# Performance work log

Measured on AMD Instinct MI355X. Metric: run time of the kernel, lower is better.

The kernel has to match this reference:

```python
import jax, jax.numpy as jnp
import numpy as np

B, H, W = 32, 128, 128
NA = 9            # number of anchors
STRIDE = 16.0
CLS_THRESH = 0.95
MAX_IOU = 0.1
NUM_PROP = 10
NEG = -1e9        # sentinel for suppressed / below-threshold scores


def setup_inputs() -> dict:
    key = jax.random.key(0)
    inputs = jax.random.normal(key, (B, H, W, NA * 4 + NA + 1), dtype=jnp.float32)
    anchors = jnp.array([[0.5, 32.0], [1.0, 32.0], [2.0, 32.0],
                         [0.5, 64.0], [1.0, 64.0], [2.0, 64.0],
                         [0.5, 128.0], [1.0, 128.0], [2.0, 128.0]], dtype=jnp.float32)
    return {"inputs": inputs, "anchors": anchors}


def _decode(inputs, anchors):
    b, h, w, c = inputs.shape
    cls = inputs[..., -1]
    # zero out 1-pixel border (the tf.pad'ed cancel matrix)
    border = jnp.zeros((h, w), inputs.dtype).at[1:-1, 1:-1].set(1.0)
    cls = cls * border
    a_reg = inputs[..., -10:-1]           # [B,H,W,9]
    bbox_reg = inputs[..., :-10]          # [B,H,W,36]
    a_idx = jnp.argmax(a_reg, axis=-1)    # [B,H,W] best anchor per position
    # gather the 4 deltas of the chosen anchor: channels a_idx*4 .. a_idx*4+3
    gidx = a_idx[..., None] * 4 + jnp.arange(4)
    deltas = jnp.take_along_axis(bbox_reg, gidx, axis=-1)          # [B,H,W,4]
    anc = anchors[a_idx].astype(jnp.float32)                       # [B,H,W,2]
    # anchor box: center x from column, center y from row, height=anc[:,1], width=anc[:,1]/anc[:,0]
    ax = (jnp.arange(w, dtype=jnp.float32)[None, :] + 0.5) * STRIDE  # [1,W]
    ay = (jnp.arange(h, dtype=jnp.float32)[:, None] + 0.5) * STRIDE  # [H,1]
    a0 = jnp.broadcast_to(ax, (h, w))[None]                          # [1,H,W]
    a1 = jnp.broadcast_to(ay, (h, w))[None]
    a2 = anc[..., 1]
    a3 = anc[..., 1] / anc[..., 0]
    b0 = deltas[..., 0] * a2 + a0
    b1 = deltas[..., 1] * a3 + a1
    b2 = jnp.exp(deltas[..., 2]) * a2
    b3 = jnp.exp(deltas[..., 3]) * a3
    bboxes = jnp.stack([b0, b1, b2, b3], axis=-1)                    # [B,H,W,4]
    coords = jnp.stack([b1 - b3 / 2, b0 - b2 / 2,
                        b1 + b3 / 2, b0 + b2 / 2], axis=-1)          # [y1,x1,y2,x2]
    scores = jnp.where(cls > CLS_THRESH, cls, NEG)                   # mask below-threshold
    n = h * w
    return (bboxes.reshape(b, n, 4), coords.reshape(b, n, 4), scores.reshape(b, n))


def _nms_one(boxes, coords, scores):
    # greedy NMS, equivalent to tf.image.non_max_suppression over the valid candidates
    n = scores.shape[0]
    area = jnp.maximum(coords[:, 2] - coords[:, 0], 0.0) * jnp.maximum(coords[:, 3] - coords[:, 1], 0.0)
    idx_range = jnp.arange(n)

    def body(i, state):
        sc, out = state
        j = jnp.argmax(sc)
        ok = sc[j] > NEG / 2
        sel = coords[j]
        iy1 = jnp.maximum(coords[:, 0], sel[0])
        ix1 = jnp.maximum(coords[:, 1], sel[1])
        iy2 = jnp.minimum(coords[:, 2], sel[2])
        ix2 = jnp.minimum(coords[:, 3], sel[3])
        inter = jnp.maximum(iy2 - iy1, 0.0) * jnp.maximum(ix2 - ix1, 0.0)
        area_s = jnp.maximum(sel[2] - sel[0], 0.0) * jnp.maximum(sel[3] - sel[1], 0.0)
        iou = inter / (area + area_s - inter + 1e-10)
        suppress = (iou > MAX_IOU) | (idx_range == j)
        sc = jnp.where(ok & suppress, NEG, sc)
        out = out.at[i].set(jnp.where(ok, boxes[j], jnp.zeros(4, boxes.dtype)))
        return sc, out

    out0 = jnp.zeros((NUM_PROP, 4), boxes.dtype)
    _, out = jax.lax.fori_loop(0, NUM_PROP, body, (scores, out0))
    return out


def _forward(inputs, anchors):
    bboxes, coords, scores = _decode(inputs, anchors)
    return jax.vmap(_nms_one)(bboxes, coords, scores)   # [B, NUM_PROP, 4]


def reference(inputs, anchors):
    return _forward(inputs, anchors)
```

## Files before the change

### kernel.cpp

```cpp
#include <hip/hip_runtime.h>
#include <math.h>

#define BB 32
#define HH 128
#define WW 128
#define NA 9
#define CCH 46
#define NPIX (HH*WW)
#define STRIDE_F 16.0f
#define CLS_T 0.95f
#define MAX_IOU_F 0.1f
#define NUM_PROP 10
#define NEGV -1000000000.0f

#define TILE_PIX 256
#define TILE_FLOATS (TILE_PIX * CCH)
#define TILE_VEC (TILE_FLOATS / 4)
#define TILES_PER_B (NPIX / TILE_PIX)

#define NSHARD 8
#define NREG (BB * NSHARD)
#define MAXPER 20
#define MMAX (MAXPER * 256)

__global__ __launch_bounds__(256) void decode_kernel(
    const float* __restrict__ in, const float* __restrict__ anchors,
    char* __restrict__ counters, float* __restrict__ sc_comp,
    float4* __restrict__ co_comp, float4* __restrict__ bx_comp, int capS)
{
  __shared__ float s_in[TILE_FLOATS];

  int tid = threadIdx.x;
  int tile = blockIdx.x;
  int g0 = tile * TILE_PIX;

  const float4* src = (const float4*)(in + (size_t)g0 * CCH);
  float4* dst = (float4*)s_in;
  float4 tmp[12];
#pragma unroll
  for (int i = 0; i < 12; ++i) {
    int k = tid + i * 256;
    if (k < TILE_VEC) tmp[i] = src[k];
  }
#pragma unroll
  for (int i = 0; i < 12; ++i) {
    int k = tid + i * 256;
    if (k < TILE_VEC) dst[k] = tmp[i];
  }
  __syncthreads();

  int b = tile >> 6;
  int shard = tile & (NSHARD - 1);
  int region = b * NSHARD + shard;

  int g = g0 + tid;
  int p = g & (NPIX - 1);
  int h = p >> 7;
  int w = p & (WW - 1);
  const float* px = s_in + tid * CCH;

  float cls = px[45];
  bool interior = (h >= 1) && (h <= HH - 2) && (w >= 1) && (w <= WW - 2);
  bool cand = interior && (cls > CLS_T);

  unsigned long long mask = __ballot(cand);
  if (!cand) return;

  int ai = 0; float av = px[36];
#pragma unroll
  for (int c = 1; c < NA; ++c) { float v = px[36 + c]; if (v > av) { av = v; ai = c; } }

  float d0 = px[ai * 4 + 0], d1 = px[ai * 4 + 1];
  float d2 = px[ai * 4 + 2], d3 = px[ai * 4 + 3];
  float ratio = anchors[ai * 2 + 0], sz = anchors[ai * 2 + 1];
  float a2 = sz, a3 = sz / ratio;
  float ax = ((float)w + 0.5f) * STRIDE_F;
  float ay = ((float)h + 0.5f) * STRIDE_F;
  float b0 = d0 * a2 + ax;
  float b1 = d1 * a3 + ay;
  float b2 = expf(d2) * a2;
  float b3 = expf(d3) * a3;
  float4 box = make_float4(b0, b1, b2, b3);
  float4 co  = make_float4(b1 - 0.5f * b3, b0 - 0.5f * b2,
                           b1 + 0.5f * b3, b0 + 0.5f * b2);

  int lane = tid & 63;
  int prefix = __popcll(mask & ((1ull << lane) - 1ull));
  int leader = __ffsll((unsigned long long)mask) - 1;
  int total = __popcll(mask);
  int base = 0;
  int* cnt = (int*)(counters + (size_t)region * 128);
  if (lane == leader) base = atomicAdd(cnt, total);
  base = __shfl(base, leader);
  int slot = base + prefix;
  if (slot < capS) {
    size_t gi = (size_t)region * capS + slot;
    sc_comp[gi] = cls;
    co_comp[gi] = co;
    bx_comp[gi] = box;
  }
}

__global__ __launch_bounds__(256) void nms_kernel(
    const char* __restrict__ counters, const float* __restrict__ sc_comp,
    const float4* __restrict__ co_comp, const float4* __restrict__ bx_comp,
    float* __restrict__ out, int capS)
{
  __shared__ int   s_off[NSHARD + 1];
  __shared__ float s_rv[4];
  __shared__ int   s_rk[4];
  __shared__ int   s_rgi[4];
  __shared__ float s_rc[4][4];
  __shared__ float s_ra[4];
  __shared__ float s_jv;
  __shared__ int   s_jk;
  __shared__ int   s_jgi;
  __shared__ float s_selc[4];
  __shared__ float s_area;

  int b = blockIdx.x, tid = threadIdx.x;

  if (tid == 0) {
    int acc = 0;
    s_off[0] = 0;
#pragma unroll
    for (int s = 0; s < NSHARD; ++s) {
      int c = *(const int*)(counters + (size_t)(b * NSHARD + s) * 128);
      if (c > capS) c = capS;
      acc += c;
      s_off[s + 1] = acc;
    }
  }
  __syncthreads();
  int M = s_off[NSHARD];
  if (M > MMAX) M = MMAX;

  float  sc[MAXPER];
  float4 co[MAXPER];
  float  ar[MAXPER];
  int    gidx[MAXPER];
#pragma unroll
  for (int r = 0; r < MAXPER; ++r) {
    int k = r * 256 + tid;
    if (k < M) {
      int s = 0;
#pragma unroll
      for (int t = 1; t < NSHARD; ++t) if (k >= s_off[t]) s = t;
      int gi = (b * NSHARD + s) * capS + (k - s_off[s]);
      sc[r] = sc_comp[gi];
      co[r] = co_comp[gi];
      ar[r] = fmaxf(co[r].z - co[r].x, 0.f) * fmaxf(co[r].w - co[r].y, 0.f);
      gidx[r] = gi;
    } else {
      sc[r] = NEGV; co[r] = make_float4(0.f, 0.f, 0.f, 0.f); ar[r] = 0.f; gidx[r] = 0;
    }
  }

  for (int it = 0; it < NUM_PROP; ++it) {
    float bv = -INFINITY; int bk = 0x7fffffff; int bgi = 0;
    float4 bc = make_float4(0.f, 0.f, 0.f, 0.f); float ba = 0.f;
#pragma unroll
    for (int r = 0; r < MAXPER; ++r) {
      if (sc[r] > bv) { bv = sc[r]; bk = r * 256 + tid; bgi = gidx[r]; bc = co[r]; ba = ar[r]; }
    }
    for (int off = 32; off > 0; off >>= 1) {
      float ov = __shfl_down(bv, off);
      int   ok_ = __shfl_down(bk, off);
      int   og = __shfl_down(bgi, off);
      float ocx = __shfl_down(bc.x, off), ocy = __shfl_down(bc.y, off);
      float ocz = __shfl_down(bc.z, off), ocw = __shfl_down(bc.w, off);
      float oa = __shfl_down(ba, off);
      if (ov > bv || (ov == bv && ok_ < bk)) {
        bv = ov; bk = ok_; bgi = og; ba = oa;
        bc.x = ocx; bc.y = ocy; bc.z = ocz; bc.w = ocw;
      }
    }
    int wv = tid >> 6;
    if ((tid & 63) == 0) {
      s_rv[wv] = bv; s_rk[wv] = bk; s_rgi[wv] = bgi;
      s_rc[wv][0] = bc.x; s_rc[wv][1] = bc.y; s_rc[wv][2] = bc.z; s_rc[wv][3] = bc.w;
      s_ra[wv] = ba;
    }
    __syncthreads();
    if (tid == 0) {
      float fv = s_rv[0]; int fk = s_rk[0]; int fw = 0;
#pragma unroll
      for (int q = 1; q < 4; ++q) {
        if (s_rv[q] > fv || (s_rv[q] == fv && s_rk[q] < fk)) { fv = s_rv[q]; fk = s_rk[q]; fw = q; }
      }
      s_jv = fv; s_jk = fk; s_jgi = s_rgi[fw];
      s_selc[0] = s_rc[fw][0]; s_selc[1] = s_rc[fw][1];
      s_selc[2] = s_rc[fw][2]; s_selc[3] = s_rc[fw][3];
      s_area = s_ra[fw];
    }
    __syncthreads();
    float jv = s_jv;
    bool okq = jv > (NEGV * 0.5f);

    if (okq) {
      int jk = s_jk;
      float sy1 = s_selc[0], sx1 = s_selc[1], sy2 = s_selc[2], sx2 = s_selc[3];
      float sarea = s_area;
#pragma unroll
      for (int r = 0; r < MAXPER; ++r) {
        float4 c = co[r];
        float iy1 = fmaxf(c.x, sy1);
        float ix1 = fmaxf(c.y, sx1);
        float iy2 = fminf(c.z, sy2);
        float ix2 = fminf(c.w, sx2);
        float inter = fmaxf(iy2 - iy1, 0.f) * fmaxf(ix2 - ix1, 0.f);
        float iou = inter / (ar[r] + sarea - inter + 1e-10f);
        if (iou > MAX_IOU_F || (r * 256 + tid) == jk) sc[r] = NEGV;
      }
      if (tid == 0) {
        float4 bx = bx_comp[s_jgi];
        float* o = out + (size_t)(b * NUM_PROP + it) * 4;
        o[0] = bx.x; o[1] = bx.y; o[2] = bx.z; o[3] = bx.w;
      }
    } else if (tid == 0) {
      float* o = out + (size_t)(b * NUM_PROP + it) * 4;
      o[0] = 0.f; o[1] = 0.f; o[2] = 0.f; o[3] = 0.f;
    }
    __syncthreads();
  }
}

extern "C" void kernel_launch(void* const* d_in, const int* in_sizes, int n_in,
                              void* d_out, int out_size, void* d_ws, size_t ws_size,
                              hipStream_t stream) {
  const float* in      = (const float*)d_in[0];
  const float* anchors = (const float*)d_in[1];
  float* out = (float*)d_out;

  char* ws = (char*)d_ws;
  size_t cnt_bytes = (size_t)NREG * 128;
  size_t avail = (ws_size > cnt_bytes) ? (ws_size - cnt_bytes) : 0;
  long long capS_ll = (long long)(avail / ((size_t)NREG * 36));
  int capS = (int)((capS_ll > 1024) ? 1024 : capS_ll);
  if (capS < 1) capS = 1;

  float4* co_comp = (float4*)(ws + cnt_bytes);
  size_t co_bytes = (size_t)NREG * capS * 16;
  float4* bx_comp = (float4*)(ws + cnt_bytes + co_bytes);
  float*  sc_comp = (float*)(ws + cnt_bytes + 2 * co_bytes);

  hipMemsetAsync(ws, 0, cnt_bytes, stream);

  decode_kernel<<<(BB * NPIX) / TILE_PIX, 256, 0, stream>>>(
      in, anchors, ws, sc_comp, co_comp, bx_comp, capS);
  nms_kernel<<<BB, 256, 0, stream>>>(
      ws, sc_comp, co_comp, bx_comp, out, capS);
}
```

Measured before the change: 209.5 us.

## Load tiles via global_load_lds and reconstruct output boxes from coords

The decode kernel now copies each input tile straight into LDS with the global_load_lds builtin, so the data no longer passes through registers. It also stops writing a separate box array. NMS rebuilds the output center and size from the selected corner coordinates, which saves workspace writes and a dependent global read per proposal. Launch bounds hints are added for occupancy. Reconstructing the box from coords can differ from the reference in floating-point rounding.

```diff
diff --git a/kernel.cpp b/kernel.cpp
--- a/kernel.cpp
+++ b/kernel.cpp
@@ -16,17 +16,21 @@
 #define TILE_PIX 256
 #define TILE_FLOATS (TILE_PIX * CCH)
 #define TILE_VEC (TILE_FLOATS / 4)
-#define TILES_PER_B (NPIX / TILE_PIX)
 
 #define NSHARD 8
 #define NREG (BB * NSHARD)
 #define MAXPER 20
 #define MMAX (MAXPER * 256)
 
-__global__ __launch_bounds__(256) void decode_kernel(
+#define GLL16(gp, lp)                                                          \
+  __builtin_amdgcn_global_load_lds(                                            \
+      (__attribute__((address_space(1))) void*)(gp),                           \
+      (__attribute__((address_space(3))) void*)(lp), 16, 0, 0)
+
+__global__ __launch_bounds__(256, 3) void decode_kernel(
     const float* __restrict__ in, const float* __restrict__ anchors,
     char* __restrict__ counters, float* __restrict__ sc_comp,
-    float4* __restrict__ co_comp, float4* __restrict__ bx_comp, int capS)
+    float4* __restrict__ co_comp, int capS)
 {
   __shared__ float s_in[TILE_FLOATS];
 
@@ -34,18 +38,13 @@
   int tile = blockIdx.x;
   int g0 = tile * TILE_PIX;
 
-  const float4* src = (const float4*)(in + (size_t)g0 * CCH);
-  float4* dst = (float4*)s_in;
-  float4 tmp[12];
+  const float4* srcv = (const float4*)(in + (size_t)g0 * CCH);
+  float4* dstv = (float4*)s_in;
 #pragma unroll
   for (int i = 0; i < 12; ++i) {
     int k = tid + i * 256;
-    if (k < TILE_VEC) tmp[i] = src[k];
-  }
-#pragma unroll
-  for (int i = 0; i < 12; ++i) {
-    int k = tid + i * 256;
-    if (k < TILE_VEC) dst[k] = tmp[i];
+    if (k < TILE_VEC)
+      GLL16(srcv + k, dstv + k);
   }
   __syncthreads();
 
@@ -80,9 +79,8 @@
   float b1 = d1 * a3 + ay;
   float b2 = expf(d2) * a2;
   float b3 = expf(d3) * a3;
-  float4 box = make_float4(b0, b1, b2, b3);
-  float4 co  = make_float4(b1 - 0.5f * b3, b0 - 0.5f * b2,
-                           b1 + 0.5f * b3, b0 + 0.5f * b2);
+  float4 co = make_float4(b1 - 0.5f * b3, b0 - 0.5f * b2,
+                          b1 + 0.5f * b3, b0 + 0.5f * b2);
 
   int lane = tid & 63;
   int prefix = __popcll(mask & ((1ull << lane) - 1ull));
@@ -97,24 +95,20 @@
     size_t gi = (size_t)region * capS + slot;
     sc_comp[gi] = cls;
     co_comp[gi] = co;
-    bx_comp[gi] = box;
   }
 }
 
-__global__ __launch_bounds__(256) void nms_kernel(
+__global__ __launch_bounds__(256, 1) void nms_kernel(
     const char* __restrict__ counters, const float* __restrict__ sc_comp,
-    const float4* __restrict__ co_comp, const float4* __restrict__ bx_comp,
-    float* __restrict__ out, int capS)
+    const float4* __restrict__ co_comp, float* __restrict__ out, int capS)
 {
   __shared__ int   s_off[NSHARD + 1];
   __shared__ float s_rv[4];
   __shared__ int   s_rk[4];
-  __shared__ int   s_rgi[4];
   __shared__ float s_rc[4][4];
   __shared__ float s_ra[4];
   __shared__ float s_jv;
   __shared__ int   s_jk;
-  __shared__ int   s_jgi;
   __shared__ float s_selc[4];
   __shared__ float s_area;
 
@@ -138,7 +132,6 @@
   float  sc[MAXPER];
   float4 co[MAXPER];
   float  ar[MAXPER];
-  int    gidx[MAXPER];
 #pragma unroll
   for (int r = 0; r < MAXPER; ++r) {
     int k = r * 256 + tid;
@@ -150,34 +143,32 @@
       sc[r] = sc_comp[gi];
       co[r] = co_comp[gi];
       ar[r] = fmaxf(co[r].z - co[r].x, 0.f) * fmaxf(co[r].w - co[r].y, 0.f);
-      gidx[r] = gi;
     } else {
-      sc[r] = NEGV; co[r] = make_float4(0.f, 0.f, 0.f, 0.f); ar[r] = 0.f; gidx[r] = 0;
+      sc[r] = NEGV; co[r] = make_float4(0.f, 0.f, 0.f, 0.f); ar[r] = 0.f;
     }
   }
 
   for (int it = 0; it < NUM_PROP; ++it) {
-    float bv = -INFINITY; int bk = 0x7fffffff; int bgi = 0;
+    float bv = -INFINITY; int bk = 0x7fffffff;
     float4 bc = make_float4(0.f, 0.f, 0.f, 0.f); float ba = 0.f;
 #pragma unroll
     for (int r = 0; r < MAXPER; ++r) {
-      if (sc[r] > bv) { bv = sc[r]; bk = r * 256 + tid; bgi = gidx[r]; bc = co[r]; ba = ar[r]; }
+      if (sc[r] > bv) { bv = sc[r]; bk = r * 256 + tid; bc = co[r]; ba = ar[r]; }
     }
     for (int off = 32; off > 0; off >>= 1) {
       float ov = __shfl_down(bv, off);
       int   ok_ = __shfl_down(bk, off);
-      int   og = __shfl_down(bgi, off);
       float ocx = __shfl_down(bc.x, off), ocy = __shfl_down(bc.y, off);
       float ocz = __shfl_down(bc.z, off), ocw = __shfl_down(bc.w, off);
       float oa = __shfl_down(ba, off);
       if (ov > bv || (ov == bv && ok_ < bk)) {
-        bv = ov; bk = ok_; bgi = og; ba = oa;
+        bv = ov; bk = ok_; ba = oa;
         bc.x = ocx; bc.y = ocy; bc.z = ocz; bc.w = ocw;
       }
     }
     int wv = tid >> 6;
     if ((tid & 63) == 0) {
-      s_rv[wv] = bv; s_rk[wv] = bk; s_rgi[wv] = bgi;
+      s_rv[wv] = bv; s_rk[wv] = bk;
       s_rc[wv][0] = bc.x; s_rc[wv][1] = bc.y; s_rc[wv][2] = bc.z; s_rc[wv][3] = bc.w;
       s_ra[wv] = ba;
     }
@@ -188,7 +179,7 @@
       for (int q = 1; q < 4; ++q) {
         if (s_rv[q] > fv || (s_rv[q] == fv && s_rk[q] < fk)) { fv = s_rv[q]; fk = s_rk[q]; fw = q; }
       }
-      s_jv = fv; s_jk = fk; s_jgi = s_rgi[fw];
+      s_jv = fv; s_jk = fk;
       s_selc[0] = s_rc[fw][0]; s_selc[1] = s_rc[fw][1];
       s_selc[2] = s_rc[fw][2]; s_selc[3] = s_rc[fw][3];
       s_area = s_ra[fw];
@@ -213,9 +204,11 @@
         if (iou > MAX_IOU_F || (r * 256 + tid) == jk) sc[r] = NEGV;
       }
       if (tid == 0) {
-        float4 bx = bx_comp[s_jgi];
         float* o = out + (size_t)(b * NUM_PROP + it) * 4;
-        o[0] = bx.x; o[1] = bx.y; o[2] = bx.z; o[3] = bx.w;
+        o[0] = 0.5f * (sx1 + sx2);
+        o[1] = 0.5f * (sy1 + sy2);
+        o[2] = sx2 - sx1;
+        o[3] = sy2 - sy1;
       }
     } else if (tid == 0) {
       float* o = out + (size_t)(b * NUM_PROP + it) * 4;
@@ -235,19 +228,18 @@
   char* ws = (char*)d_ws;
   size_t cnt_bytes = (size_t)NREG * 128;
   size_t avail = (ws_size > cnt_bytes) ? (ws_size - cnt_bytes) : 0;
-  long long capS_ll = (long long)(avail / ((size_t)NREG * 36));
+  long long capS_ll = (long long)(avail / ((size_t)NREG * 20));
   int capS = (int)((capS_ll > 1024) ? 1024 : capS_ll);
   if (capS < 1) capS = 1;
 
   float4* co_comp = (float4*)(ws + cnt_bytes);
   size_t co_bytes = (size_t)NREG * capS * 16;
-  float4* bx_comp = (float4*)(ws + cnt_bytes + co_bytes);
-  float*  sc_comp = (float*)(ws + cnt_bytes + 2 * co_bytes);
+  float*  sc_comp = (float*)(ws + cnt_bytes + co_bytes);
 
   hipMemsetAsync(ws, 0, cnt_bytes, stream);
 
   decode_kernel<<<(BB * NPIX) / TILE_PIX, 256, 0, stream>>>(
-      in, anchors, ws, sc_comp, co_comp, bx_comp, capS);
+      in, anchors, ws, sc_comp, co_comp, capS);
   nms_kernel<<<BB, 256, 0, stream>>>(
-      ws, sc_comp, co_comp, bx_comp, out, capS);
+      ws, sc_comp, co_comp, out, capS);
 }
```

Measured after the change: 177.8 us. -15.1%, faster.
